# Performance work log

Measured on AMD Instinct MI355X. Metric: run time of the kernel, lower is better.

## Reference

```python
import jax, jax.numpy as jnp
import numpy as np

B, HF, WF = 4, 64, 64   # fine (output) resolution
HC, WC = 32, 32         # coarse resolution
CF = 256                # fine channels
CC = 256                # coarse channels (DCN input)
F = 256                 # filters
DG, K, KK = 8, 3, 9     # deformable groups, kernel
OFFS = DG * 2 * KK      # 144 offset channels
MASKS = DG * KK         # 72 mask channels
PAD = 1                 # 'same' padding for k=3, dil=1


def setup_inputs() -> dict:
    key = jax.random.key(0)
    ks = jax.random.split(key, 8)
    rn = lambda k, s, sc: jax.random.normal(k, s, jnp.float32) * sc
    return {
        "fine": rn(ks[0], (B, HF, WF, CF), 1.0),
        "coarse": rn(ks[1], (B, HC, WC, CC), 1.0),
        "fs_attn_w": rn(ks[2], (CF, CF), (2.0 / CF) ** 0.5),
        "fs_conv_w": rn(ks[3], (CF, F), (2.0 / CF) ** 0.5),
        "offset_w": rn(ks[4], (F + CC, 2 * F), (2.0 / (F + CC)) ** 0.5),
        "om_w": rn(ks[5], (K, K, 2 * F, OFFS + MASKS), 0.01),  # original is zero-init; small random for nontrivial offsets
        "om_b": jnp.zeros((OFFS + MASKS,), jnp.float32),
        "dcn_kernel": rn(ks[6], (KK * CC, F), 1.0 / np.sqrt(KK * CC)),
        "dcn_bias": jnp.zeros((F,), jnp.float32),
    }


def _dcn_columns(x, offset, mask):
    # x: [B,H,W,C]; offset: [B,H,W,DG,KK,2] (dy,dx); mask: [B,H,W,DG,KK]
    Bx, H, W, C = x.shape
    Cg = C // DG
    xg = x.reshape(Bx, H, W, DG, Cg)
    dt = x.dtype
    ky, kx = jnp.meshgrid(jnp.arange(K), jnp.arange(K), indexing="ij")
    tap_y = (ky.reshape(-1) - PAD).astype(dt)  # [KK]
    tap_x = (kx.reshape(-1) - PAD).astype(dt)
    # fractional sample positions, stride 1 / dilation 1
    py = (jnp.arange(H, dtype=dt)[None, :, None, None, None]
          + tap_y[None, None, None, None, :] + offset[..., 0])  # [B,H,W,DG,KK]
    px = (jnp.arange(W, dtype=dt)[None, None, :, None, None]
          + tap_x[None, None, None, None, :] + offset[..., 1])
    y0 = jnp.floor(py); x0 = jnp.floor(px)
    wy1 = py - y0; wx1 = px - x0
    wy0 = 1.0 - wy1; wx0 = 1.0 - wx1
    y0i = y0.astype(jnp.int32); x0i = x0.astype(jnp.int32)
    bi = jnp.arange(Bx).reshape(Bx, 1, 1, 1, 1)
    gi = jnp.arange(DG).reshape(1, 1, 1, DG, 1)

    def gather(yi, xi):
        valid = (yi >= 0) & (yi < H) & (xi >= 0) & (xi < W)
        yc = jnp.clip(yi, 0, H - 1)
        xc = jnp.clip(xi, 0, W - 1)
        v = xg[bi, yc, xc, gi]  # [B,H,W,DG,KK,Cg]
        return v * valid.astype(dt)[..., None]

    val = (gather(y0i, x0i) * (wy0 * wx0)[..., None]
           + gather(y0i, x0i + 1) * (wy0 * wx1)[..., None]
           + gather(y0i + 1, x0i) * (wy1 * wx0)[..., None]
           + gather(y0i + 1, x0i + 1) * (wy1 * wx1)[..., None])
    val = val * mask[..., None]  # modulation
    # column layout: tap-major, then channel (g*Cg + cg), matching kernel [KK*C, F]
    cols = jnp.transpose(val, (0, 1, 2, 4, 3, 5)).reshape(Bx, H, W, KK * C)
    return cols


def reference(fine, coarse, fs_attn_w, fs_conv_w, offset_w, om_w, om_b,
              dcn_kernel, dcn_bias):
    # 1) upsample coarse to fine resolution (half-pixel bilinear)
    coarse_up = jax.image.resize(coarse, (B, HF, WF, CC), "bilinear")
    # 2) FeatureSelection: GAP -> 1x1 sigmoid attention -> x*(a+1) -> 1x1 conv
    gap = jnp.mean(fine, axis=(1, 2), keepdims=True)
    attn = jax.nn.sigmoid(jnp.einsum("bhwc,cd->bhwd", gap, fs_attn_w))
    fine_cal = jnp.einsum("bhwc,cf->bhwf", fine * (attn + 1.0), fs_conv_w)
    # 3) offset features from concat(fine_cal, 2*coarse_up) via 1x1 conv
    fc = jnp.concatenate([fine_cal, coarse_up * 2.0], axis=-1)
    align = jnp.einsum("bhwc,cf->bhwf", fc, offset_w)
    # 4) DCNv2: offset/mask predictor conv (3x3 same)
    om = jax.lax.conv_general_dilated(
        align, om_w, (1, 1), "SAME",
        dimension_numbers=("NHWC", "HWIO", "NHWC")) + om_b
    offset = om[..., :OFFS].reshape(B, HF, WF, DG, KK, 2)
    mask = (jax.nn.sigmoid(om[..., OFFS:]) * 2.0).reshape(B, HF, WF, DG, KK)
    # 5) modulated deformable im2col + matmul + bias
    cols = _dcn_columns(coarse_up, offset, mask)
    out = cols @ dcn_kernel + dcn_bias
    # 6) activation + residual with selected fine features
    return jax.nn.relu(out) + fine_cal
```

## Files before the change

### kernel.cpp

```cpp
#include <hip/hip_runtime.h>
#include <hip/hip_bf16.h>

using u16 = unsigned short;
typedef __attribute__((ext_vector_type(8))) short short8;
typedef __attribute__((ext_vector_type(4))) float floatx4;

__device__ __forceinline__ float b2f(u16 u) {
    union { unsigned int i; float f; } v; v.i = ((unsigned int)u) << 16; return v.f;
}
__device__ __forceinline__ u16 f2b(float f) {
    __hip_bfloat16 h = __float2bfloat16(f);
    u16 u; __builtin_memcpy(&u, &h, sizeof(u)); return u;
}


__global__ __launch_bounds__(256) void k_gap(const float* __restrict__ fine,
                                             float* __restrict__ gap) {
    int b = blockIdx.y, chunk = blockIdx.x, c = threadIdx.x;
    const float* p = fine + ((size_t)b * 4096 + (size_t)chunk * 128) * 256 + c;
    float s = 0.f;
    for (int i = 0; i < 128; i++) s += p[(size_t)i * 256];
    atomicAdd(&gap[b * 256 + c], s);
}

__global__ __launch_bounds__(256) void k_attn(const float* __restrict__ gap,
                                              const float* __restrict__ w,
                                              float* __restrict__ a1) {
    int b = blockIdx.x, d = threadIdx.x;
    float s = 0.f;
    for (int c = 0; c < 256; c++) s += gap[b * 256 + c] * w[c * 256 + d];
    s *= (1.0f / 4096.0f);
    a1[b * 256 + d] = 1.0f + 1.0f / (1.0f + expf(-s));
}

__global__ __launch_bounds__(256) void k_upsample(const float* __restrict__ coarse,
                                                  u16* __restrict__ fcu) {
    int tid = threadIdx.x;
    int p = blockIdx.x * 32 + (tid >> 3);
    int ch = (tid & 7) * 32;
    int b = p >> 12, y = (p & 4095) >> 6, x = p & 63;
    float sy = fminf(fmaxf(0.5f * y - 0.25f, 0.0f), 31.0f);
    float sx = fminf(fmaxf(0.5f * x - 0.25f, 0.0f), 31.0f);
    int y0 = (int)floorf(sy); float wy = sy - (float)y0; int y1 = min(y0 + 1, 31);
    int x0 = (int)floorf(sx); float wx = sx - (float)x0; int x1 = min(x0 + 1, 31);
    float w00 = (1.f - wy) * (1.f - wx), w01 = (1.f - wy) * wx;
    float w10 = wy * (1.f - wx), w11 = wy * wx;
    const float* c00 = coarse + ((size_t)((b * 32 + y0) * 32 + x0)) * 256 + ch;
    const float* c01 = coarse + ((size_t)((b * 32 + y0) * 32 + x1)) * 256 + ch;
    const float* c10 = coarse + ((size_t)((b * 32 + y1) * 32 + x0)) * 256 + ch;
    const float* c11 = coarse + ((size_t)((b * 32 + y1) * 32 + x1)) * 256 + ch;
    u16* dst = fcu + (size_t)p * 512 + 256 + ch;
    #pragma unroll
    for (int k = 0; k < 4; k++) {
        float4 a0 = *(const float4*)(c00 + k * 8), a1v = *(const float4*)(c00 + k * 8 + 4);
        float4 b0 = *(const float4*)(c01 + k * 8), b1v = *(const float4*)(c01 + k * 8 + 4);
        float4 g0 = *(const float4*)(c10 + k * 8), g1 = *(const float4*)(c10 + k * 8 + 4);
        float4 d0 = *(const float4*)(c11 + k * 8), d1 = *(const float4*)(c11 + k * 8 + 4);
        u16 o[8] = {
            f2b(w00 * a0.x + w01 * b0.x + w10 * g0.x + w11 * d0.x),
            f2b(w00 * a0.y + w01 * b0.y + w10 * g0.y + w11 * d0.y),
            f2b(w00 * a0.z + w01 * b0.z + w10 * g0.z + w11 * d0.z),
            f2b(w00 * a0.w + w01 * b0.w + w10 * g0.w + w11 * d0.w),
            f2b(w00 * a1v.x + w01 * b1v.x + w10 * g1.x + w11 * d1.x),
            f2b(w00 * a1v.y + w01 * b1v.y + w10 * g1.y + w11 * d1.y),
            f2b(w00 * a1v.z + w01 * b1v.z + w10 * g1.z + w11 * d1.z),
            f2b(w00 * a1v.w + w01 * b1v.w + w10 * g1.w + w11 * d1.w)};
        uint4 ov; __builtin_memcpy(&ov, o, 16);
        *(uint4*)(dst + k * 8) = ov;
    }
}

__global__ __launch_bounds__(256) void k_wswz(const float* __restrict__ fsw,
                                              const float* __restrict__ Wk,
                                              const float* __restrict__ omw,
                                              u16* __restrict__ wb0,
                                              u16* __restrict__ wkt,
                                              u16* __restrict__ bomw) {
    int bx = blockIdx.x;
    int tid = threadIdx.x;
    if (bx < 32) {
        int idx = bx * 256 + tid;
        int lane = idx & 63, nt = (idx >> 6) & 15, ks = idx >> 10;
        int n = nt * 16 + (lane & 15);
        int k0 = ks * 32 + (lane >> 4) * 8;
        u16 tmp[8];
        #pragma unroll
        for (int j = 0; j < 8; j++) tmp[j] = f2b(fsw[(size_t)(k0 + j) * 256 + n]);
        uint4 v; __builtin_memcpy(&v, tmp, 16);
        *(uint4*)(wb0 + (size_t)idx * 8) = v;
    } else if (bx < 320) {
        int idx = (bx - 32) * 256 + tid;
        int lane = idx & 63, nt = (idx >> 6) & 15, ks = idx >> 10;
        int n = nt * 16 + (lane & 15);
        int k0 = ks * 32 + (lane >> 4) * 8;
        u16 tmp[8];
        #pragma unroll
        for (int j = 0; j < 8; j++) tmp[j] = f2b(Wk[(size_t)(k0 + j) * 256 + n]);
        uint4 v; __builtin_memcpy(&v, tmp, 16);
        *(uint4*)(wkt + (size_t)idx * 8) = v;
    } else {
        int idx = (bx - 320) * 256 + tid;
        int lane = idx & 63, nt = (idx >> 6) & 15, ks = (idx >> 10) & 15, t = idx >> 14;
        int n = nt * 16 + (lane & 15);
        int f0 = ks * 32 + (lane >> 4) * 8;
        u16 tmp[8];
        #pragma unroll
        for (int j = 0; j < 8; j++)
            tmp[j] = (n < 216) ? f2b(omw[((size_t)t * 512 + f0 + j) * 216 + n]) : (u16)0;
        uint4 v; __builtin_memcpy(&v, tmp, 16);
        *(uint4*)(bomw + (size_t)idx * 8) = v;
    }
}

__global__ __launch_bounds__(256) void k_g0(const float* __restrict__ fine,
                                            const float* __restrict__ a1,
                                            const u16* __restrict__ wb,
                                            u16* __restrict__ fcu) {
    __shared__ u16 cols[32 * 264];
    int tid = threadIdx.x;
    int m0 = blockIdx.x * 32;
    int lane = tid & 63, wid = tid >> 6;
    int r = lane & 15, quad = lane >> 4;
    int sp = tid >> 3, coff = (tid & 7) * 32;
    int row = m0 + sp;
    int b = row >> 12;
    {
        const float* src = fine + (size_t)row * 256 + coff;
        const float* ap = a1 + b * 256 + coff;
        u16* dst = &cols[sp * 264 + coff];
        #pragma unroll
        for (int ch = 0; ch < 4; ch++) {
            float4 v0 = *(const float4*)(src + ch * 8);
            float4 v1 = *(const float4*)(src + ch * 8 + 4);
            float4 s0 = *(const float4*)(ap + ch * 8);
            float4 s1 = *(const float4*)(ap + ch * 8 + 4);
            u16 o[8] = {f2b(v0.x * s0.x), f2b(v0.y * s0.y), f2b(v0.z * s0.z), f2b(v0.w * s0.w),
                        f2b(v1.x * s1.x), f2b(v1.y * s1.y), f2b(v1.z * s1.z), f2b(v1.w * s1.w)};
            uint4 ov; __builtin_memcpy(&ov, o, 16);
            *(uint4*)(dst + ch * 8) = ov;
        }
    }
    __syncthreads();
    floatx4 acc[2][4];
    #pragma unroll
    for (int i = 0; i < 2; i++)
        #pragma unroll
        for (int j = 0; j < 4; j++) acc[i][j] = (floatx4){0.f, 0.f, 0.f, 0.f};
    #pragma unroll
    for (int ks = 0; ks < 8; ks++) {
        short8 a0 = *(const short8*)&cols[r * 264 + ks * 32 + quad * 8];
        short8 a1v = *(const short8*)&cols[(16 + r) * 264 + ks * 32 + quad * 8];
        const u16* bp = wb + (((size_t)ks * 16 + wid * 4) * 64 + lane) * 8;
        short8 b0 = *(const short8*)(bp);
        short8 b1 = *(const short8*)(bp + 512);
        short8 b2 = *(const short8*)(bp + 1024);
        short8 b3 = *(const short8*)(bp + 1536);
        acc[0][0] = __builtin_amdgcn_mfma_f32_16x16x32_bf16(a0, b0, acc[0][0], 0, 0, 0);
        acc[0][1] = __builtin_amdgcn_mfma_f32_16x16x32_bf16(a0, b1, acc[0][1], 0, 0, 0);
        acc[0][2] = __builtin_amdgcn_mfma_f32_16x16x32_bf16(a0, b2, acc[0][2], 0, 0, 0);
        acc[0][3] = __builtin_amdgcn_mfma_f32_16x16x32_bf16(a0, b3, acc[0][3], 0, 0, 0);
        acc[1][0] = __builtin_amdgcn_mfma_f32_16x16x32_bf16(a1v, b0, acc[1][0], 0, 0, 0);
        acc[1][1] = __builtin_amdgcn_mfma_f32_16x16x32_bf16(a1v, b1, acc[1][1], 0, 0, 0);
        acc[1][2] = __builtin_amdgcn_mfma_f32_16x16x32_bf16(a1v, b2, acc[1][2], 0, 0, 0);
        acc[1][3] = __builtin_amdgcn_mfma_f32_16x16x32_bf16(a1v, b3, acc[1][3], 0, 0, 0);
    }
    #pragma unroll
    for (int mt = 0; mt < 2; mt++)
        #pragma unroll
        for (int nt = 0; nt < 4; nt++) {
            int f = wid * 64 + nt * 16 + r;
            #pragma unroll
            for (int reg = 0; reg < 4; reg++) {
                int pp = m0 + mt * 16 + quad * 4 + reg;
                fcu[(size_t)pp * 512 + f] = f2b(acc[mt][nt][reg]);
            }
        }
}

__global__ __launch_bounds__(256) void k_weff(const float* __restrict__ ow,
                                              const u16* __restrict__ bomw,
                                              u16* __restrict__ wtf) {
    __shared__ u16 cols[32 * 520];
    int tid = threadIdx.x;
    int c0 = blockIdx.x * 32, t = blockIdx.y;
    int lane = tid & 63, wid = tid >> 6;
    int r = lane & 15, quad = lane >> 4;
    int sp = tid >> 3, f0 = (tid & 7) * 64;
    {
        const float* src = ow + (size_t)(c0 + sp) * 512 + f0;
        u16* dst = &cols[sp * 520 + f0];
        #pragma unroll
        for (int k = 0; k < 8; k++) {
            float4 v0 = *(const float4*)(src + k * 8);
            float4 v1 = *(const float4*)(src + k * 8 + 4);
            u16 o[8] = {f2b(v0.x), f2b(v0.y), f2b(v0.z), f2b(v0.w),
                        f2b(v1.x), f2b(v1.y), f2b(v1.z), f2b(v1.w)};
            uint4 ov; __builtin_memcpy(&ov, o, 16);
            *(uint4*)(dst + k * 8) = ov;
        }
    }
    __syncthreads();
    floatx4 acc[2][4];
    #pragma unroll
    for (int i = 0; i < 2; i++)
        #pragma unroll
        for (int j = 0; j < 4; j++) acc[i][j] = (floatx4){0.f, 0.f, 0.f, 0.f};
    #pragma unroll
    for (int ks = 0; ks < 16; ks++) {
        short8 a0 = *(const short8*)&cols[r * 520 + ks * 32 + quad * 8];
        short8 a1v = *(const short8*)&cols[(16 + r) * 520 + ks * 32 + quad * 8];
        const u16* bp = bomw + (((size_t)(t * 16 + ks) * 16 + wid * 4) * 64 + lane) * 8;
        short8 b0 = *(const short8*)(bp);
        short8 b1 = *(const short8*)(bp + 512);
        short8 b2 = *(const short8*)(bp + 1024);
        short8 b3 = *(const short8*)(bp + 1536);
        acc[0][0] = __builtin_amdgcn_mfma_f32_16x16x32_bf16(a0, b0, acc[0][0], 0, 0, 0);
        acc[0][1] = __builtin_amdgcn_mfma_f32_16x16x32_bf16(a0, b1, acc[0][1], 0, 0, 0);
        acc[0][2] = __builtin_amdgcn_mfma_f32_16x16x32_bf16(a0, b2, acc[0][2], 0, 0, 0);
        acc[0][3] = __builtin_amdgcn_mfma_f32_16x16x32_bf16(a0, b3, acc[0][3], 0, 0, 0);
        acc[1][0] = __builtin_amdgcn_mfma_f32_16x16x32_bf16(a1v, b0, acc[1][0], 0, 0, 0);
        acc[1][1] = __builtin_amdgcn_mfma_f32_16x16x32_bf16(a1v, b1, acc[1][1], 0, 0, 0);
        acc[1][2] = __builtin_amdgcn_mfma_f32_16x16x32_bf16(a1v, b2, acc[1][2], 0, 0, 0);
        acc[1][3] = __builtin_amdgcn_mfma_f32_16x16x32_bf16(a1v, b3, acc[1][3], 0, 0, 0);
    }
    #pragma unroll
    for (int mt = 0; mt < 2; mt++) {
        #pragma unroll
        for (int nt = 0; nt < 4; nt++) {
            int n = wid * 64 + nt * 16 + r;
            #pragma unroll
            for (int reg = 0; reg < 4; reg++) {
                int c = c0 + mt * 16 + quad * 4 + reg;
                float sc = (c >= 256) ? 2.0f : 1.0f;
                size_t addr = (((size_t)(t * 16 + (c >> 5)) * 16 + (n >> 4)) * 64
                               + ((c >> 3) & 3) * 16 + (n & 15)) * 8 + (c & 7);
                wtf[addr] = f2b(acc[mt][nt][reg] * sc);
            }
        }
    }
}

__global__ __launch_bounds__(256, 2) void k_conv(const u16* __restrict__ fcu,
                                                 const u16* __restrict__ wtf,
                                                 const float* __restrict__ bias,
                                                 float* __restrict__ om) {
    __shared__ u16 halo[2][100 * 40];
    int tid = threadIdx.x;
    int bx = blockIdx.x;
    int xcd = bx & 7, i = bx >> 3;
    int prow = xcd * 4 + (i >> 4);
    int pcol = (i >> 1) & 7;
    int ns = i & 1;
    int b = prow >> 3;
    int py0 = (prow & 7) * 8, px0 = pcol * 8;
    int n0 = ns * 128;
    int lane = tid & 63, wid = tid >> 6;
    int r = lane & 15, quad = lane >> 4;

    int j0 = tid, j1 = tid + 256;
    int pix0 = j0 >> 2, q80 = j0 & 3;
    int pix1 = j1 >> 2, q81 = j1 & 3;
    int hy0 = pix0 / 10, hx0 = pix0 - hy0 * 10;
    int hy1 = pix1 / 10, hx1 = pix1 - hy1 * 10;
    int gy0 = py0 - 1 + hy0, gx0 = px0 - 1 + hx0;
    int gy1 = py0 - 1 + hy1, gx1 = px0 - 1 + hx1;
    bool act1 = j1 < 400;
    bool in0 = gy0 >= 0 && gy0 < 64 && gx0 >= 0 && gx0 < 64;
    bool in1 = act1 && gy1 >= 0 && gy1 < 64 && gx1 >= 0 && gx1 < 64;
    const u16* gs0 = fcu + ((size_t)((b * 64 + min(max(gy0, 0), 63)) * 64 + min(max(gx0, 0), 63))) * 512 + q80 * 8;
    const u16* gs1 = fcu + ((size_t)((b * 64 + min(max(gy1, 0), 63)) * 64 + min(max(gx1, 0), 63))) * 512 + q81 * 8;
    int ld0 = pix0 * 40 + q80 * 8;
    int ld1 = pix1 * 40 + q81 * 8;

    floatx4 acc[4][2];
    #pragma unroll
    for (int a = 0; a < 4; a++)
        #pragma unroll
        for (int c = 0; c < 2; c++) acc[a][c] = (floatx4){0.f, 0.f, 0.f, 0.f};

    {
        uint4 v0 = make_uint4(0, 0, 0, 0), v1 = make_uint4(0, 0, 0, 0);
        if (in0) v0 = *(const uint4*)(gs0);
        if (in1) v1 = *(const uint4*)(gs1);
        *(uint4*)&halo[0][ld0] = v0;
        if (act1) *(uint4*)&halo[0][ld1] = v1;
    }
    __syncthreads();

    for (int cq = 0; cq < 16; cq++) {
        int cur = cq & 1;
        const u16* hb = &halo[cur][0];
        short8 Bp[2][2];
        #pragma unroll
        for (int d = 0; d < 2; d++) {
            const u16* bp = wtf + (((size_t)(d * 16 + cq) * 16 + ns * 8 + wid * 2) * 64 + lane) * 8;
            Bp[d][0] = *(const short8*)(bp);
            Bp[d][1] = *(const short8*)(bp + 512);
        }
        uint4 v0 = make_uint4(0, 0, 0, 0), v1 = make_uint4(0, 0, 0, 0);
        #pragma unroll
        for (int t = 0; t < 7; t++) {
            int d = t & 1;
            short8 b0 = Bp[d][0], b1 = Bp[d][1];
            const u16* bp = wtf + (((size_t)((t + 2) * 16 + cq) * 16 + ns * 8 + wid * 2) * 64 + lane) * 8;
            Bp[d][0] = *(const short8*)(bp);
            Bp[d][1] = *(const short8*)(bp + 512);
            int dy = t / 3 - 1, dx = t - (t / 3) * 3 - 1;
            short8 a[4];
            #pragma unroll
            for (int mt = 0; mt < 4; mt++) {
                int m = mt * 16 + r;
                int hy = (m >> 3) + 1 + dy, hx = (m & 7) + 1 + dx;
                a[mt] = *(const short8*)&hb[(hy * 10 + hx) * 40 + quad * 8];
            }
            #pragma unroll
            for (int mt = 0; mt < 4; mt++) {
                acc[mt][0] = __builtin_amdgcn_mfma_f32_16x16x32_bf16(a[mt], b0, acc[mt][0], 0, 0, 0);
                acc[mt][1] = __builtin_amdgcn_mfma_f32_16x16x32_bf16(a[mt], b1, acc[mt][1], 0, 0, 0);
            }
        }
        if (cq < 15) {
            if (in0) v0 = *(const uint4*)(gs0 + (cq + 1) * 32);
            if (in1) v1 = *(const uint4*)(gs1 + (cq + 1) * 32);
        }
        #pragma unroll
        for (int t = 7; t < 9; t++) {
            int d = t & 1;
            short8 b0 = Bp[d][0], b1 = Bp[d][1];
            int dy = t / 3 - 1, dx = t - (t / 3) * 3 - 1;
            short8 a[4];
            #pragma unroll
            for (int mt = 0; mt < 4; mt++) {
                int m = mt * 16 + r;
                int hy = (m >> 3) + 1 + dy, hx = (m & 7) + 1 + dx;
                a[mt] = *(const short8*)&hb[(hy * 10 + hx) * 40 + quad * 8];
            }
            #pragma unroll
            for (int mt = 0; mt < 4; mt++) {
                acc[mt][0] = __builtin_amdgcn_mfma_f32_16x16x32_bf16(a[mt], b0, acc[mt][0], 0, 0, 0);
                acc[mt][1] = __builtin_amdgcn_mfma_f32_16x16x32_bf16(a[mt], b1, acc[mt][1], 0, 0, 0);
            }
        }
        if (cq < 15) {
            *(uint4*)&halo[cur ^ 1][ld0] = v0;
            if (act1) *(uint4*)&halo[cur ^ 1][ld1] = v1;
        }
        __syncthreads();
    }
    #pragma unroll
    for (int nt = 0; nt < 2; nt++) {
        int n = n0 + wid * 32 + nt * 16 + r;
        if (n < 216) {
            float bv = bias[n];
            #pragma unroll
            for (int mt = 0; mt < 4; mt++) {
                #pragma unroll
                for (int reg = 0; reg < 4; reg++) {
                    int m = mt * 16 + quad * 4 + reg;
                    int gyy = py0 + (m >> 3), gxx = px0 + (m & 7);
                    size_t pix = (size_t)((b * 64 + gyy) * 64 + gxx);
                    om[pix * 216 + n] = acc[mt][nt][reg] + bv;
                }
            }
        }
    }
}

struct Smp { uint4 g[4][4]; float w[4]; };

__device__ __forceinline__ void dcn_issue(Smp& s, const u16* __restrict__ cub,
                                          int y, int xs, int sg, int t,
                                          float oy, float ox, float mlog) {
    int dy = t / 3 - 1, dx = t - (t / 3) * 3 - 1;
    float mk = 2.0f / (1.0f + expf(-mlog));
    float py = (float)(y + dy) + oy;
    float px = (float)(xs + dx) + ox;
    float fy = floorf(py), fx = floorf(px);
    int iy = (int)fy, ix = (int)fx;
    float wy1 = py - fy, wx1 = px - fx;
    float wy0 = 1.f - wy1, wx0 = 1.f - wx1;
    bool y0in = iy >= 0 && iy < 64, y1in = iy >= -1 && iy < 63;
    bool x0in = ix >= 0 && ix < 64, x1in = ix >= -1 && ix < 63;
    s.w[0] = (y0in && x0in) ? wy0 * wx0 * mk : 0.f;
    s.w[1] = (y0in && x1in) ? wy0 * wx1 * mk : 0.f;
    s.w[2] = (y1in && x0in) ? wy1 * wx0 * mk : 0.f;
    s.w[3] = (y1in && x1in) ? wy1 * wx1 * mk : 0.f;
    int iy0 = min(max(iy, 0), 63), iy1 = min(max(iy + 1, 0), 63);
    int ix0 = min(max(ix, 0), 63), ix1 = min(max(ix + 1, 0), 63);
    const u16* p00 = cub + (size_t)(iy0 * 64 + ix0) * 512 + sg * 32;
    const u16* p01 = cub + (size_t)(iy0 * 64 + ix1) * 512 + sg * 32;
    const u16* p10 = cub + (size_t)(iy1 * 64 + ix0) * 512 + sg * 32;
    const u16* p11 = cub + (size_t)(iy1 * 64 + ix1) * 512 + sg * 32;
    #pragma unroll
    for (int k = 0; k < 4; k++) {
        s.g[0][k] = *(const uint4*)(p00 + k * 8);
        s.g[1][k] = *(const uint4*)(p01 + k * 8);
        s.g[2][k] = *(const uint4*)(p10 + k * 8);
        s.g[3][k] = *(const uint4*)(p11 + k * 8);
    }
}

__device__ __forceinline__ void dcn_blend(const Smp& s, u16* __restrict__ dst) {
    #pragma unroll
    for (int k = 0; k < 4; k++) {
        const u16* p00 = (const u16*)&s.g[0][k];
        const u16* p01 = (const u16*)&s.g[1][k];
        const u16* p10 = (const u16*)&s.g[2][k];
        const u16* p11 = (const u16*)&s.g[3][k];
        u16 o[8];
        #pragma unroll
        for (int j = 0; j < 8; j++) {
            float v = s.w[0] * b2f(p00[j]) + s.w[1] * b2f(p01[j])
                    + s.w[2] * b2f(p10[j]) + s.w[3] * b2f(p11[j]);
            o[j] = f2b(v);
        }
        uint4 ov; __builtin_memcpy(&ov, o, 16);
        *(uint4*)(dst + k * 8) = ov;
    }
}

__global__ __launch_bounds__(256, 2) void k_dcn(const u16* __restrict__ fcu,
                                                const float* __restrict__ om,
                                                const u16* __restrict__ bfr,
                                                const float* __restrict__ bias,
                                                float* __restrict__ out) {
    __shared__ u16 cols[32 * 776];
    int tid = threadIdx.x;
    int bx = blockIdx.x;
    int xcd = bx & 7, i = bx >> 3;
    int grow = xcd * 32 + (i >> 1);
    int p0 = grow * 64 + (i & 1) * 32;
    int b = p0 >> 12;
    int y = (p0 & 4095) >> 6;
    int x0 = p0 & 63;
    int lane = tid & 63, wid = tid >> 6;
    int r = lane & 15, quad = lane >> 4;
    int sp = tid >> 3, sg = tid & 7;
    int pix = p0 + sp;
    int xs = x0 + sp;
    const u16* cub = fcu + ((size_t)b * 4096) * 512 + 256;
    const float* omp = om + (size_t)pix * 216;
    u16* mydst = &cols[0] + sp * 776 + sg * 32;

    float offy[9], offx[9], ml[9];
    #pragma unroll
    for (int t = 0; t < 9; t++) {
        offy[t] = omp[sg * 18 + 2 * t];
        offx[t] = omp[sg * 18 + 2 * t + 1];
        ml[t] = omp[144 + sg * 9 + t];
    }

    floatx4 acc[2][4];
    #pragma unroll
    for (int a = 0; a < 2; a++)
        #pragma unroll
        for (int c = 0; c < 4; c++) acc[a][c] = (floatx4){0.f, 0.f, 0.f, 0.f};

    #pragma unroll
    for (int g = 0; g < 3; g++) {
        int t0 = g * 3, t1 = g * 3 + 1, t2 = g * 3 + 2;
        Smp s0, s1;
        dcn_issue(s0, cub, y, xs, sg, t0, offy[t0], offx[t0], ml[t0]);
        dcn_issue(s1, cub, y, xs, sg, t1, offy[t1], offx[t1], ml[t1]);
        dcn_blend(s0, mydst + 0 * 256);
        dcn_issue(s0, cub, y, xs, sg, t2, offy[t2], offx[t2], ml[t2]);
        dcn_blend(s1, mydst + 1 * 256);
        dcn_blend(s0, mydst + 2 * 256);
        __syncthreads();
        short8 Bb[4][4];
        #pragma unroll
        for (int d = 0; d < 4; d++) {
            const u16* bp = bfr + (((size_t)(g * 24 + d) * 16 + wid * 4) * 64 + lane) * 8;
            Bb[d][0] = *(const short8*)(bp);
            Bb[d][1] = *(const short8*)(bp + 512);
            Bb[d][2] = *(const short8*)(bp + 1024);
            Bb[d][3] = *(const short8*)(bp + 1536);
        }
        #pragma unroll
        for (int ksl = 0; ksl < 24; ksl++) {
            int d = ksl & 3;
            short8 b0 = Bb[d][0], b1 = Bb[d][1], b2 = Bb[d][2], b3 = Bb[d][3];
            if (ksl + 4 < 24) {
                const u16* bp = bfr + (((size_t)(g * 24 + ksl + 4) * 16 + wid * 4) * 64 + lane) * 8;
                Bb[d][0] = *(const short8*)(bp);
                Bb[d][1] = *(const short8*)(bp + 512);
                Bb[d][2] = *(const short8*)(bp + 1024);
                Bb[d][3] = *(const short8*)(bp + 1536);
            }
            short8 a0 = *(const short8*)&cols[r * 776 + ksl * 32 + quad * 8];
            short8 a1 = *(const short8*)&cols[(16 + r) * 776 + ksl * 32 + quad * 8];
            acc[0][0] = __builtin_amdgcn_mfma_f32_16x16x32_bf16(a0, b0, acc[0][0], 0, 0, 0);
            acc[0][1] = __builtin_amdgcn_mfma_f32_16x16x32_bf16(a0, b1, acc[0][1], 0, 0, 0);
            acc[0][2] = __builtin_amdgcn_mfma_f32_16x16x32_bf16(a0, b2, acc[0][2], 0, 0, 0);
            acc[0][3] = __builtin_amdgcn_mfma_f32_16x16x32_bf16(a0, b3, acc[0][3], 0, 0, 0);
            acc[1][0] = __builtin_amdgcn_mfma_f32_16x16x32_bf16(a1, b0, acc[1][0], 0, 0, 0);
            acc[1][1] = __builtin_amdgcn_mfma_f32_16x16x32_bf16(a1, b1, acc[1][1], 0, 0, 0);
            acc[1][2] = __builtin_amdgcn_mfma_f32_16x16x32_bf16(a1, b2, acc[1][2], 0, 0, 0);
            acc[1][3] = __builtin_amdgcn_mfma_f32_16x16x32_bf16(a1, b3, acc[1][3], 0, 0, 0);
        }
        __syncthreads();
    }
    #pragma unroll
    for (int mt = 0; mt < 2; mt++) {
        #pragma unroll
        for (int nt = 0; nt < 4; nt++) {
            int f = wid * 64 + nt * 16 + r;
            float bv = bias[f];
            #pragma unroll
            for (int reg = 0; reg < 4; reg++) {
                int pp = p0 + mt * 16 + quad * 4 + reg;
                float fcv = b2f(fcu[(size_t)pp * 512 + f]);
                out[(size_t)pp * 256 + f] = fmaxf(acc[mt][nt][reg] + bv, 0.f) + fcv;
            }
        }
    }
}

extern "C" void kernel_launch(void* const* d_in, const int* in_sizes, int n_in,
                              void* d_out, int out_size, void* d_ws, size_t ws_size,
                              hipStream_t stream) {
    const float* fine       = (const float*)d_in[0];
    const float* coarse     = (const float*)d_in[1];
    const float* fs_attn_w  = (const float*)d_in[2];
    const float* fs_conv_w  = (const float*)d_in[3];
    const float* offset_w   = (const float*)d_in[4];
    const float* om_w       = (const float*)d_in[5];
    const float* om_b       = (const float*)d_in[6];
    const float* dcn_kernel = (const float*)d_in[7];
    const float* dcn_bias   = (const float*)d_in[8];
    float* out = (float*)d_out;

    char* ws = (char*)d_ws;
    size_t off = 0;
    float* gap = (float*)(ws + off); off += 4096;
    float* a1  = (float*)(ws + off); off += 4096;
    u16*   fcu = (u16*)(ws + off);   off += 16777216ull;
    float* om  = (float*)(ws + off); off += 14155776ull;
    u16*   wtf = (u16*)(ws + off);   off += 2359296ull;
    u16*   wkt = (u16*)(ws + off);   off += 1179648ull;
    u16*   wb0 = (u16*)(ws + off);   off += 131072ull;
    u16*   bomw = (u16*)(ws + off);  off += 2359296ull;

    hipMemsetAsync(gap, 0, 4 * 256 * sizeof(float), stream);
    k_gap<<<dim3(32, 4), 256, 0, stream>>>(fine, gap);
    k_attn<<<4, 256, 0, stream>>>(gap, fs_attn_w, a1);
    k_upsample<<<512, 256, 0, stream>>>(coarse, fcu);
    k_wswz<<<896, 256, 0, stream>>>(fs_conv_w, dcn_kernel, om_w, wb0, wkt, bomw);
    k_g0<<<512, 256, 0, stream>>>(fine, a1, wb0, fcu);
    k_weff<<<dim3(16, 9), 256, 0, stream>>>(offset_w, bomw, wtf);
    k_conv<<<512, 256, 0, stream>>>(fcu, wtf, om_b, om);
    k_dcn<<<512, 256, 0, stream>>>(fcu, om, wkt, dcn_bias, out);
}
```

Before: 248.1 us.

## Halve DCN pixel tile to 16 and double grid for more occupancy

Each k_dcn block now handles 16 pixels instead of 32. Each thread samples half a deformable group's channels (16 instead of 32), and the grid doubles to 1024 blocks with launch bounds raised to 4 blocks per CU. The aim is more waves to hide the latency of the scattered bilinear gathers, plus smaller LDS and register use. In exchange, every block re-reads the full DCN weight matrix for half as many pixels, so weight traffic per output doubles and MFMA reuse of each B fragment halves.

Measured after the change: 258.8 us. 4.3% more time.

```diff
diff --git a/kernel.cpp b/kernel.cpp
--- a/kernel.cpp
+++ b/kernel.cpp
@@ -366,11 +366,11 @@
     }
 }
 
-struct Smp { uint4 g[4][4]; float w[4]; };
-
-__device__ __forceinline__ void dcn_issue(Smp& s, const u16* __restrict__ cub,
-                                          int y, int xs, int sg, int t,
-                                          float oy, float ox, float mlog) {
+struct SmpH { uint4 g[4][2]; float w[4]; };
+
+__device__ __forceinline__ void dcn_issue_h(SmpH& s, const u16* __restrict__ cub,
+                                            int y, int xs, int ch0, int t,
+                                            float oy, float ox, float mlog) {
     int dy = t / 3 - 1, dx = t - (t / 3) * 3 - 1;
     float mk = 2.0f / (1.0f + expf(-mlog));
     float py = (float)(y + dy) + oy;
@@ -387,12 +387,12 @@
     s.w[3] = (y1in && x1in) ? wy1 * wx1 * mk : 0.f;
     int iy0 = min(max(iy, 0), 63), iy1 = min(max(iy + 1, 0), 63);
     int ix0 = min(max(ix, 0), 63), ix1 = min(max(ix + 1, 0), 63);
-    const u16* p00 = cub + (size_t)(iy0 * 64 + ix0) * 512 + sg * 32;
-    const u16* p01 = cub + (size_t)(iy0 * 64 + ix1) * 512 + sg * 32;
-    const u16* p10 = cub + (size_t)(iy1 * 64 + ix0) * 512 + sg * 32;
-    const u16* p11 = cub + (size_t)(iy1 * 64 + ix1) * 512 + sg * 32;
-    #pragma unroll
-    for (int k = 0; k < 4; k++) {
+    const u16* p00 = cub + (size_t)(iy0 * 64 + ix0) * 512 + ch0;
+    const u16* p01 = cub + (size_t)(iy0 * 64 + ix1) * 512 + ch0;
+    const u16* p10 = cub + (size_t)(iy1 * 64 + ix0) * 512 + ch0;
+    const u16* p11 = cub + (size_t)(iy1 * 64 + ix1) * 512 + ch0;
+    #pragma unroll
+    for (int k = 0; k < 2; k++) {
         s.g[0][k] = *(const uint4*)(p00 + k * 8);
         s.g[1][k] = *(const uint4*)(p01 + k * 8);
         s.g[2][k] = *(const uint4*)(p10 + k * 8);
@@ -400,9 +400,9 @@
     }
 }
 
-__device__ __forceinline__ void dcn_blend(const Smp& s, u16* __restrict__ dst) {
-    #pragma unroll
-    for (int k = 0; k < 4; k++) {
+__device__ __forceinline__ void dcn_blend_h(const SmpH& s, u16* __restrict__ dst) {
+    #pragma unroll
+    for (int k = 0; k < 2; k++) {
         const u16* p00 = (const u16*)&s.g[0][k];
         const u16* p01 = (const u16*)&s.g[1][k];
         const u16* p10 = (const u16*)&s.g[2][k];
@@ -419,58 +419,59 @@
     }
 }
 
-__global__ __launch_bounds__(256, 2) void k_dcn(const u16* __restrict__ fcu,
+__global__ __launch_bounds__(256, 4) void k_dcn(const u16* __restrict__ fcu,
                                                 const float* __restrict__ om,
                                                 const u16* __restrict__ bfr,
                                                 const float* __restrict__ bias,
                                                 float* __restrict__ out) {
-    __shared__ u16 cols[32 * 776];
+    __shared__ u16 cols[16 * 776];
     int tid = threadIdx.x;
     int bx = blockIdx.x;
     int xcd = bx & 7, i = bx >> 3;
-    int grow = xcd * 32 + (i >> 1);
-    int p0 = grow * 64 + (i & 1) * 32;
+    int grow = xcd * 32 + (i >> 2);
+    int p0 = grow * 64 + (i & 3) * 16;
     int b = p0 >> 12;
     int y = (p0 & 4095) >> 6;
     int x0 = p0 & 63;
     int lane = tid & 63, wid = tid >> 6;
     int r = lane & 15, quad = lane >> 4;
-    int sp = tid >> 3, sg = tid & 7;
+    int sp = tid >> 4;
+    int sgh = tid & 15;
+    int g = sgh >> 1, h = sgh & 1;
+    int ch0 = g * 32 + h * 16;
     int pix = p0 + sp;
     int xs = x0 + sp;
     const u16* cub = fcu + ((size_t)b * 4096) * 512 + 256;
     const float* omp = om + (size_t)pix * 216;
-    u16* mydst = &cols[0] + sp * 776 + sg * 32;
+    u16* mydst = &cols[0] + sp * 776 + ch0;
 
     float offy[9], offx[9], ml[9];
     #pragma unroll
     for (int t = 0; t < 9; t++) {
-        offy[t] = omp[sg * 18 + 2 * t];
-        offx[t] = omp[sg * 18 + 2 * t + 1];
-        ml[t] = omp[144 + sg * 9 + t];
-    }
-
-    floatx4 acc[2][4];
-    #pragma unroll
-    for (int a = 0; a < 2; a++)
-        #pragma unroll
-        for (int c = 0; c < 4; c++) acc[a][c] = (floatx4){0.f, 0.f, 0.f, 0.f};
-
-    #pragma unroll
-    for (int g = 0; g < 3; g++) {
-        int t0 = g * 3, t1 = g * 3 + 1, t2 = g * 3 + 2;
-        Smp s0, s1;
-        dcn_issue(s0, cub, y, xs, sg, t0, offy[t0], offx[t0], ml[t0]);
-        dcn_issue(s1, cub, y, xs, sg, t1, offy[t1], offx[t1], ml[t1]);
-        dcn_blend(s0, mydst + 0 * 256);
-        dcn_issue(s0, cub, y, xs, sg, t2, offy[t2], offx[t2], ml[t2]);
-        dcn_blend(s1, mydst + 1 * 256);
-        dcn_blend(s0, mydst + 2 * 256);
+        offy[t] = omp[g * 18 + 2 * t];
+        offx[t] = omp[g * 18 + 2 * t + 1];
+        ml[t] = omp[144 + g * 9 + t];
+    }
+
+    floatx4 acc[4];
+    #pragma unroll
+    for (int c = 0; c < 4; c++) acc[c] = (floatx4){0.f, 0.f, 0.f, 0.f};
+
+    #pragma unroll
+    for (int g3 = 0; g3 < 3; g3++) {
+        int t0 = g3 * 3, t1 = g3 * 3 + 1, t2 = g3 * 3 + 2;
+        SmpH s0, s1;
+        dcn_issue_h(s0, cub, y, xs, ch0, t0, offy[t0], offx[t0], ml[t0]);
+        dcn_issue_h(s1, cub, y, xs, ch0, t1, offy[t1], offx[t1], ml[t1]);
+        dcn_blend_h(s0, mydst + 0 * 256);
+        dcn_issue_h(s0, cub, y, xs, ch0, t2, offy[t2], offx[t2], ml[t2]);
+        dcn_blend_h(s1, mydst + 1 * 256);
+        dcn_blend_h(s0, mydst + 2 * 256);
         __syncthreads();
         short8 Bb[4][4];
         #pragma unroll
         for (int d = 0; d < 4; d++) {
-            const u16* bp = bfr + (((size_t)(g * 24 + d) * 16 + wid * 4) * 64 + lane) * 8;
+            const u16* bp = bfr + (((size_t)(g3 * 24 + d) * 16 + wid * 4) * 64 + lane) * 8;
             Bb[d][0] = *(const short8*)(bp);
             Bb[d][1] = *(const short8*)(bp + 512);
             Bb[d][2] = *(const short8*)(bp + 1024);
@@ -481,37 +482,29 @@
             int d = ksl & 3;
             short8 b0 = Bb[d][0], b1 = Bb[d][1], b2 = Bb[d][2], b3 = Bb[d][3];
             if (ksl + 4 < 24) {
-                const u16* bp = bfr + (((size_t)(g * 24 + ksl + 4) * 16 + wid * 4) * 64 + lane) * 8;
+                const u16* bp = bfr + (((size_t)(g3 * 24 + ksl + 4) * 16 + wid * 4) * 64 + lane) * 8;
                 Bb[d][0] = *(const short8*)(bp);
                 Bb[d][1] = *(const short8*)(bp + 512);
                 Bb[d][2] = *(const short8*)(bp + 1024);
                 Bb[d][3] = *(const short8*)(bp + 1536);
             }
             short8 a0 = *(const short8*)&cols[r * 776 + ksl * 32 + quad * 8];
-            short8 a1 = *(const short8*)&cols[(16 + r) * 776 + ksl * 32 + quad * 8];
-            acc[0][0] = __builtin_amdgcn_mfma_f32_16x16x32_bf16(a0, b0, acc[0][0], 0, 0, 0);
-            acc[0][1] = __builtin_amdgcn_mfma_f32_16x16x32_bf16(a0, b1, acc[0][1], 0, 0, 0);
-            acc[0][2] = __builtin_amdgcn_mfma_f32_16x16x32_bf16(a0, b2, acc[0][2], 0, 0, 0);
-            acc[0][3] = __builtin_amdgcn_mfma_f32_16x16x32_bf16(a0, b3, acc[0][3], 0, 0, 0);
-            acc[1][0] = __builtin_amdgcn_mfma_f32_16x16x32_bf16(a1, b0, acc[1][0], 0, 0, 0);
-            acc[1][1] = __builtin_amdgcn_mfma_f32_16x16x32_bf16(a1, b1, acc[1][1], 0, 0, 0);
-            acc[1][2] = __builtin_amdgcn_mfma_f32_16x16x32_bf16(a1, b2, acc[1][2], 0, 0, 0);
-            acc[1][3] = __builtin_amdgcn_mfma_f32_16x16x32_bf16(a1, b3, acc[1][3], 0, 0, 0);
+            acc[0] = __builtin_amdgcn_mfma_f32_16x16x32_bf16(a0, b0, acc[0], 0, 0, 0);
+            acc[1] = __builtin_amdgcn_mfma_f32_16x16x32_bf16(a0, b1, acc[1], 0, 0, 0);
+            acc[2] = __builtin_amdgcn_mfma_f32_16x16x32_bf16(a0, b2, acc[2], 0, 0, 0);
+            acc[3] = __builtin_amdgcn_mfma_f32_16x16x32_bf16(a0, b3, acc[3], 0, 0, 0);
         }
         __syncthreads();
     }
     #pragma unroll
-    for (int mt = 0; mt < 2; mt++) {
-        #pragma unroll
-        for (int nt = 0; nt < 4; nt++) {
-            int f = wid * 64 + nt * 16 + r;
-            float bv = bias[f];
-            #pragma unroll
-            for (int reg = 0; reg < 4; reg++) {
-                int pp = p0 + mt * 16 + quad * 4 + reg;
-                float fcv = b2f(fcu[(size_t)pp * 512 + f]);
-                out[(size_t)pp * 256 + f] = fmaxf(acc[mt][nt][reg] + bv, 0.f) + fcv;
-            }
+    for (int nt = 0; nt < 4; nt++) {
+        int f = wid * 64 + nt * 16 + r;
+        float bv = bias[f];
+        #pragma unroll
+        for (int reg = 0; reg < 4; reg++) {
+            int pp = p0 + quad * 4 + reg;
+            float fcv = b2f(fcu[(size_t)pp * 512 + f]);
+            out[(size_t)pp * 256 + f] = fmaxf(acc[nt][reg] + bv, 0.f) + fcv;
         }
     }
 }
@@ -549,5 +542,5 @@
     k_g0<<<512, 256, 0, stream>>>(fine, a1, wb0, fcu);
     k_weff<<<dim3(16, 9), 256, 0, stream>>>(offset_w, bomw, wtf);
     k_conv<<<512, 256, 0, stream>>>(fcu, wtf, om_b, om);
-    k_dcn<<<512, 256, 0, stream>>>(fcu, om, wkt, dcn_bias, out);
-}
+    k_dcn<<<1024, 256, 0, stream>>>(fcu, om, wkt, dcn_bias, out);
+}
```

## Double DCN block to 512 threads, splitting channel groups and output filters per wave

Applied to the files above, without the earlier changes.

The deformable-conv kernel now runs 512 threads per block. Each thread samples 16 channels instead of 32, and each of the 8 waves computes 32 output filters instead of 64. All 12 bilinear corner gathers for a 3-tap group are issued up front, with a sched_barrier before blending, to raise memory-level parallelism and hide gather latency. The cost is fewer accumulators per wave, with B fragments loaded by more waves, and higher per-block register pressure under launch bounds (512,2).

Result: faster. 235.5 us (-5.1%).

```diff
diff --git a/kernel.cpp b/kernel.cpp
--- a/kernel.cpp
+++ b/kernel.cpp
@@ -366,60 +366,7 @@
     }
 }
 
-struct Smp { uint4 g[4][4]; float w[4]; };
-
-__device__ __forceinline__ void dcn_issue(Smp& s, const u16* __restrict__ cub,
-                                          int y, int xs, int sg, int t,
-                                          float oy, float ox, float mlog) {
-    int dy = t / 3 - 1, dx = t - (t / 3) * 3 - 1;
-    float mk = 2.0f / (1.0f + expf(-mlog));
-    float py = (float)(y + dy) + oy;
-    float px = (float)(xs + dx) + ox;
-    float fy = floorf(py), fx = floorf(px);
-    int iy = (int)fy, ix = (int)fx;
-    float wy1 = py - fy, wx1 = px - fx;
-    float wy0 = 1.f - wy1, wx0 = 1.f - wx1;
-    bool y0in = iy >= 0 && iy < 64, y1in = iy >= -1 && iy < 63;
-    bool x0in = ix >= 0 && ix < 64, x1in = ix >= -1 && ix < 63;
-    s.w[0] = (y0in && x0in) ? wy0 * wx0 * mk : 0.f;
-    s.w[1] = (y0in && x1in) ? wy0 * wx1 * mk : 0.f;
-    s.w[2] = (y1in && x0in) ? wy1 * wx0 * mk : 0.f;
-    s.w[3] = (y1in && x1in) ? wy1 * wx1 * mk : 0.f;
-    int iy0 = min(max(iy, 0), 63), iy1 = min(max(iy + 1, 0), 63);
-    int ix0 = min(max(ix, 0), 63), ix1 = min(max(ix + 1, 0), 63);
-    const u16* p00 = cub + (size_t)(iy0 * 64 + ix0) * 512 + sg * 32;
-    const u16* p01 = cub + (size_t)(iy0 * 64 + ix1) * 512 + sg * 32;
-    const u16* p10 = cub + (size_t)(iy1 * 64 + ix0) * 512 + sg * 32;
-    const u16* p11 = cub + (size_t)(iy1 * 64 + ix1) * 512 + sg * 32;
-    #pragma unroll
-    for (int k = 0; k < 4; k++) {
-        s.g[0][k] = *(const uint4*)(p00 + k * 8);
-        s.g[1][k] = *(const uint4*)(p01 + k * 8);
-        s.g[2][k] = *(const uint4*)(p10 + k * 8);
-        s.g[3][k] = *(const uint4*)(p11 + k * 8);
-    }
-}
-
-__device__ __forceinline__ void dcn_blend(const Smp& s, u16* __restrict__ dst) {
-    #pragma unroll
-    for (int k = 0; k < 4; k++) {
-        const u16* p00 = (const u16*)&s.g[0][k];
-        const u16* p01 = (const u16*)&s.g[1][k];
-        const u16* p10 = (const u16*)&s.g[2][k];
-        const u16* p11 = (const u16*)&s.g[3][k];
-        u16 o[8];
-        #pragma unroll
-        for (int j = 0; j < 8; j++) {
-            float v = s.w[0] * b2f(p00[j]) + s.w[1] * b2f(p01[j])
-                    + s.w[2] * b2f(p10[j]) + s.w[3] * b2f(p11[j]);
-            o[j] = f2b(v);
-        }
-        uint4 ov; __builtin_memcpy(&ov, o, 16);
-        *(uint4*)(dst + k * 8) = ov;
-    }
-}
-
-__global__ __launch_bounds__(256, 2) void k_dcn(const u16* __restrict__ fcu,
+__global__ __launch_bounds__(512, 2) void k_dcn(const u16* __restrict__ fcu,
                                                 const float* __restrict__ om,
                                                 const u16* __restrict__ bfr,
                                                 const float* __restrict__ bias,
@@ -435,76 +382,118 @@
     int x0 = p0 & 63;
     int lane = tid & 63, wid = tid >> 6;
     int r = lane & 15, quad = lane >> 4;
-    int sp = tid >> 3, sg = tid & 7;
+    int sp = tid >> 4;
+    int sgh = tid & 15;
+    int g = sgh >> 1, h = sgh & 1;
+    int ch0 = g * 32 + h * 16;
     int pix = p0 + sp;
     int xs = x0 + sp;
     const u16* cub = fcu + ((size_t)b * 4096) * 512 + 256;
     const float* omp = om + (size_t)pix * 216;
-    u16* mydst = &cols[0] + sp * 776 + sg * 32;
+    u16* mydst = &cols[0] + sp * 776 + ch0;
 
     float offy[9], offx[9], ml[9];
     #pragma unroll
     for (int t = 0; t < 9; t++) {
-        offy[t] = omp[sg * 18 + 2 * t];
-        offx[t] = omp[sg * 18 + 2 * t + 1];
-        ml[t] = omp[144 + sg * 9 + t];
-    }
-
-    floatx4 acc[2][4];
+        offy[t] = omp[g * 18 + 2 * t];
+        offx[t] = omp[g * 18 + 2 * t + 1];
+        ml[t] = omp[144 + g * 9 + t];
+    }
+
+    floatx4 acc[2][2];
     #pragma unroll
     for (int a = 0; a < 2; a++)
         #pragma unroll
-        for (int c = 0; c < 4; c++) acc[a][c] = (floatx4){0.f, 0.f, 0.f, 0.f};
-
-    #pragma unroll
-    for (int g = 0; g < 3; g++) {
-        int t0 = g * 3, t1 = g * 3 + 1, t2 = g * 3 + 2;
-        Smp s0, s1;
-        dcn_issue(s0, cub, y, xs, sg, t0, offy[t0], offx[t0], ml[t0]);
-        dcn_issue(s1, cub, y, xs, sg, t1, offy[t1], offx[t1], ml[t1]);
-        dcn_blend(s0, mydst + 0 * 256);
-        dcn_issue(s0, cub, y, xs, sg, t2, offy[t2], offx[t2], ml[t2]);
-        dcn_blend(s1, mydst + 1 * 256);
-        dcn_blend(s0, mydst + 2 * 256);
+        for (int c = 0; c < 2; c++) acc[a][c] = (floatx4){0.f, 0.f, 0.f, 0.f};
+
+    #pragma unroll
+    for (int g3 = 0; g3 < 3; g3++) {
+        float w[3][4];
+        int ofs[3][4];
+        #pragma unroll
+        for (int tl = 0; tl < 3; tl++) {
+            int t = g3 * 3 + tl;
+            int dy = t / 3 - 1, dx = t - (t / 3) * 3 - 1;
+            float mk = 2.0f / (1.0f + expf(-ml[t]));
+            float py = (float)(y + dy) + offy[t];
+            float px = (float)(xs + dx) + offx[t];
+            float fy = floorf(py), fx = floorf(px);
+            int iy = (int)fy, ix = (int)fx;
+            float wy1 = py - fy, wx1 = px - fx;
+            float wy0 = 1.f - wy1, wx0 = 1.f - wx1;
+            bool y0in = iy >= 0 && iy < 64, y1in = iy >= -1 && iy < 63;
+            bool x0in = ix >= 0 && ix < 64, x1in = ix >= -1 && ix < 63;
+            w[tl][0] = (y0in && x0in) ? wy0 * wx0 * mk : 0.f;
+            w[tl][1] = (y0in && x1in) ? wy0 * wx1 * mk : 0.f;
+            w[tl][2] = (y1in && x0in) ? wy1 * wx0 * mk : 0.f;
+            w[tl][3] = (y1in && x1in) ? wy1 * wx1 * mk : 0.f;
+            int iy0 = min(max(iy, 0), 63), iy1 = min(max(iy + 1, 0), 63);
+            int ix0 = min(max(ix, 0), 63), ix1 = min(max(ix + 1, 0), 63);
+            ofs[tl][0] = (iy0 * 64 + ix0) * 512 + ch0;
+            ofs[tl][1] = (iy0 * 64 + ix1) * 512 + ch0;
+            ofs[tl][2] = (iy1 * 64 + ix0) * 512 + ch0;
+            ofs[tl][3] = (iy1 * 64 + ix1) * 512 + ch0;
+        }
+        uint4 G[3][4][2];
+        #pragma unroll
+        for (int tl = 0; tl < 3; tl++)
+            #pragma unroll
+            for (int c = 0; c < 4; c++) {
+                const u16* p = cub + ofs[tl][c];
+                G[tl][c][0] = *(const uint4*)(p);
+                G[tl][c][1] = *(const uint4*)(p + 8);
+            }
+        __builtin_amdgcn_sched_barrier(0);
+        #pragma unroll
+        for (int tl = 0; tl < 3; tl++) {
+            #pragma unroll
+            for (int k = 0; k < 2; k++) {
+                const u16* q0 = (const u16*)&G[tl][0][k];
+                const u16* q1 = (const u16*)&G[tl][1][k];
+                const u16* q2 = (const u16*)&G[tl][2][k];
+                const u16* q3 = (const u16*)&G[tl][3][k];
+                u16 o[8];
+                #pragma unroll
+                for (int j = 0; j < 8; j++) {
+                    float v = w[tl][0] * b2f(q0[j]) + w[tl][1] * b2f(q1[j])
+                            + w[tl][2] * b2f(q2[j]) + w[tl][3] * b2f(q3[j]);
+                    o[j] = f2b(v);
+                }
+                uint4 ov; __builtin_memcpy(&ov, o, 16);
+                *(uint4*)(mydst + tl * 256 + k * 8) = ov;
+            }
+        }
         __syncthreads();
-        short8 Bb[4][4];
+        short8 Bb[4][2];
         #pragma unroll
         for (int d = 0; d < 4; d++) {
-            const u16* bp = bfr + (((size_t)(g * 24 + d) * 16 + wid * 4) * 64 + lane) * 8;
+            const u16* bp = bfr + (((size_t)(g3 * 24 + d) * 16 + wid * 2) * 64 + lane) * 8;
             Bb[d][0] = *(const short8*)(bp);
             Bb[d][1] = *(const short8*)(bp + 512);
-            Bb[d][2] = *(const short8*)(bp + 1024);
-            Bb[d][3] = *(const short8*)(bp + 1536);
         }
         #pragma unroll
         for (int ksl = 0; ksl < 24; ksl++) {
             int d = ksl & 3;
-            short8 b0 = Bb[d][0], b1 = Bb[d][1], b2 = Bb[d][2], b3 = Bb[d][3];
+            short8 b0 = Bb[d][0], b1 = Bb[d][1];
             if (ksl + 4 < 24) {
-                const u16* bp = bfr + (((size_t)(g * 24 + ksl + 4) * 16 + wid * 4) * 64 + lane) * 8;
+                const u16* bp = bfr + (((size_t)(g3 * 24 + ksl + 4) * 16 + wid * 2) * 64 + lane) * 8;
                 Bb[d][0] = *(const short8*)(bp);
                 Bb[d][1] = *(const short8*)(bp + 512);
-                Bb[d][2] = *(const short8*)(bp + 1024);
-                Bb[d][3] = *(const short8*)(bp + 1536);
             }
             short8 a0 = *(const short8*)&cols[r * 776 + ksl * 32 + quad * 8];
             short8 a1 = *(const short8*)&cols[(16 + r) * 776 + ksl * 32 + quad * 8];
             acc[0][0] = __builtin_amdgcn_mfma_f32_16x16x32_bf16(a0, b0, acc[0][0], 0, 0, 0);
             acc[0][1] = __builtin_amdgcn_mfma_f32_16x16x32_bf16(a0, b1, acc[0][1], 0, 0, 0);
-            acc[0][2] = __builtin_amdgcn_mfma_f32_16x16x32_bf16(a0, b2, acc[0][2], 0, 0, 0);
-            acc[0][3] = __builtin_amdgcn_mfma_f32_16x16x32_bf16(a0, b3, acc[0][3], 0, 0, 0);
             acc[1][0] = __builtin_amdgcn_mfma_f32_16x16x32_bf16(a1, b0, acc[1][0], 0, 0, 0);
             acc[1][1] = __builtin_amdgcn_mfma_f32_16x16x32_bf16(a1, b1, acc[1][1], 0, 0, 0);
-            acc[1][2] = __builtin_amdgcn_mfma_f32_16x16x32_bf16(a1, b2, acc[1][2], 0, 0, 0);
-            acc[1][3] = __builtin_amdgcn_mfma_f32_16x16x32_bf16(a1, b3, acc[1][3], 0, 0, 0);
         }
         __syncthreads();
     }
     #pragma unroll
     for (int mt = 0; mt < 2; mt++) {
         #pragma unroll
-        for (int nt = 0; nt < 4; nt++) {
-            int f = wid * 64 + nt * 16 + r;
+        for (int nt = 0; nt < 2; nt++) {
+            int f = wid * 32 + nt * 16 + r;
             float bv = bias[f];
             #pragma unroll
             for (int reg = 0; reg < 4; reg++) {
@@ -549,5 +538,5 @@
     k_g0<<<512, 256, 0, stream>>>(fine, a1, wb0, fcu);
     k_weff<<<dim3(16, 9), 256, 0, stream>>>(offset_w, bomw, wtf);
     k_conv<<<512, 256, 0, stream>>>(fcu, wtf, om_b, om);
-    k_dcn<<<512, 256, 0, stream>>>(fcu, om, wkt, dcn_bias, out);
-}
+    k_dcn<<<512, 512, 0, stream>>>(fcu, om, wkt, dcn_bias, out);
+}
```
